# Kernel tuning notes

Hardware: AMD Instinct MI355X
Metric: run time of the kernel (lower is better)

## Reference

```python
import jax, jax.numpy as jnp
import numpy as np

D_MODEL = 1024
NUM_SLOTS = 64
TOP_K = 8
B, T = 4, 4096


def setup_inputs() -> dict:
    key = jax.random.key(0)
    ks = jax.random.split(key, 16)
    D, S = D_MODEL, NUM_SLOTS
    H = D // 2  # route MLP hidden (hardcoded d_model//2 in source)
    sc = lambda fan_in: 1.0 / np.sqrt(fan_in)
    inp = {
        "x": jax.random.normal(ks[0], (B, T, D), dtype=jnp.float32),
        # learned params
        "slot_init": jax.random.normal(ks[1], (S, D), dtype=jnp.float32) * 0.1,
        "slot_scale": jnp.ones((S, 1), dtype=jnp.float32),
        "w1": jax.random.normal(ks[2], (H, 2 * D), dtype=jnp.float32) * sc(2 * D),
        "b1": jnp.zeros((H,), dtype=jnp.float32),
        "w2": jax.random.normal(ks[3], (S, H), dtype=jnp.float32) * sc(H),
        "b2": jnp.zeros((S,), dtype=jnp.float32),
        "gru_wih": jax.random.normal(ks[4], (3 * D, D), dtype=jnp.float32) * sc(D),
        "gru_whh": jax.random.normal(ks[5], (3 * D, D), dtype=jnp.float32) * sc(D),
        "gru_bih": jnp.zeros((3 * D,), dtype=jnp.float32),
        "gru_bhh": jnp.zeros((3 * D,), dtype=jnp.float32),
        "wv": jax.random.normal(ks[6], (D, D), dtype=jnp.float32) * sc(D),
        "bv": jnp.zeros((D,), dtype=jnp.float32),
        "wo": jax.random.normal(ks[7], (D, D), dtype=jnp.float32) * sc(D),
        "bo": jnp.zeros((D,), dtype=jnp.float32),
        "tau": jnp.ones((1,), dtype=jnp.float32),
    }
    return inp


def _forward(x, slot_init, slot_scale, w1, b1, w2, b2,
             gru_wih, gru_whh, gru_bih, gru_bhh, wv, bv, wo, bo, tau):
    Bn, Tn, D = x.shape
    Sn = slot_init.shape[0]
    # initial slot states, expanded over batch: (B, S, D)
    S = jnp.broadcast_to((slot_init * slot_scale)[None], (Bn, Sn, D)).astype(x.dtype)
    slot_mean = S.mean(axis=1, keepdims=True)                      # (B,1,D)
    ctx = jnp.concatenate([x, jnp.broadcast_to(slot_mean, x.shape)], axis=-1)  # (B,T,2D)
    h = jax.nn.gelu(ctx @ w1.T + b1, approximate=False)
    route_logits = (h @ w2.T + b2) / (jnp.abs(tau) + 0.1)          # (B,T,S)
    topk_vals, topk_idx = jax.lax.top_k(route_logits, TOP_K)
    topk_w = jax.nn.softmax(topk_vals, axis=-1)                    # (B,T,K)
    # scatter top-k weights into dense alpha (B,T,S)
    alpha = jnp.sum(topk_w[..., None] * jax.nn.one_hot(topk_idx, Sn, dtype=x.dtype), axis=-2)
    slot_input = jnp.einsum('bts,btd->bsd', alpha, x)              # dispatch
    slot_wsum = alpha.sum(axis=1) + 1e-8                           # (B,S)
    gi = (slot_input / slot_wsum[..., None]).reshape(Bn * Sn, D)
    hs = S.reshape(Bn * Sn, D)
    # GRUCell (torch semantics)
    gx = gi @ gru_wih.T + gru_bih                                  # (BS, 3D)
    gh = hs @ gru_whh.T + gru_bhh
    xr, xz, xn = jnp.split(gx, 3, axis=-1)
    hr, hz, hn = jnp.split(gh, 3, axis=-1)
    r = jax.nn.sigmoid(xr + hr)
    z = jax.nn.sigmoid(xz + hz)
    n = jnp.tanh(xn + r * hn)
    h_new = (1.0 - z) * n + z * hs
    S_new = h_new.reshape(Bn, Sn, D)
    slot_values = S_new @ wv.T + bv                                # (B,S,D)
    out = jnp.einsum('bts,bsd->btd', alpha, slot_values)           # combine
    return out @ wo.T + bo


def reference(x, slot_init, slot_scale, w1, b1, w2, b2,
              gru_wih, gru_whh, gru_bih, gru_bhh, wv, bv, wo, bo, tau):
    return _forward(x, slot_init, slot_scale, w1, b1, w2, b2,
                    gru_wih, gru_whh, gru_bih, gru_bhh, wv, bv, wo, bo, tau)
```

## Files before the change

### kernel.cpp

```cpp
#include <hip/hip_runtime.h>

using u16 = unsigned short;
using u32 = unsigned int;

typedef __attribute__((ext_vector_type(8))) short bf16x8;
typedef __attribute__((ext_vector_type(4))) float f32x4;

#define NTOK 16384

constexpr size_t OFF_FLAG   = 0;
constexpr size_t OFF_FCNT   = 256;
constexpr size_t OFF_M      = 512;
constexpr size_t OFF_B1P64  = 8704;
constexpr size_t OFF_B1P32  = 12800;
constexpr size_t OFF_B2F    = 14848;
constexpr size_t OFF_BIHF   = 15104;
constexpr size_t OFF_BHHF   = 27392;
constexpr size_t OFF_BVF    = 39680;
constexpr size_t OFF_BOF    = 43776;
constexpr size_t OFF_FLAGS  = 47872;
constexpr size_t OFF_HSHI   = 113408;
constexpr size_t OFF_HSLO   = 244480;
constexpr size_t OFF_HSF    = 375552;
constexpr size_t OFF_GH     = 637696;
constexpr size_t OFF_GIHI   = 1424128;
constexpr size_t OFF_GILO   = 1948416;
constexpr size_t OFF_GX     = 2472704;
constexpr size_t OFF_SNHI   = 5618432;
constexpr size_t OFF_SNLO   = 6142720;
constexpr size_t OFF_SVHI   = 6667008;
constexpr size_t OFF_SVLO   = 7191296;
constexpr size_t OFF_SVO    = 7715584;
constexpr size_t OFF_IDX    = 8764160;
constexpr size_t OFF_WGT    = 9288448;
constexpr size_t OFF_LOGITS = 9812736;
constexpr size_t OFF_W1HI   = 14007040;
constexpr size_t OFF_W1LO   = 16104192;
constexpr size_t OFF_W2HI   = 18201344;
constexpr size_t OFF_W2LO   = 18266880;
constexpr size_t OFF_WIHHI  = 18332416;
constexpr size_t OFF_WIHLO  = 24623872;
constexpr size_t OFF_WHHHI  = 30915328;
constexpr size_t OFF_WHHLO  = 37206784;
constexpr size_t OFF_WVHI   = 43498240;
constexpr size_t OFF_WVLO   = 45595392;
constexpr size_t OFF_WOHI   = 47692544;
constexpr size_t OFF_WOLO   = 49789696;
constexpr size_t OFF_HHI    = 51886848;
constexpr size_t OFF_HLO    = 68664064;
constexpr size_t WS_NEED    = 85441280;

__device__ __forceinline__ float bf2f(u16 u) {
  union { u32 i; float f; } c; c.i = ((u32)u) << 16; return c.f;
}
__device__ __forceinline__ u16 f2bf(float f) {
  u32 x = __float_as_uint(f);
  x += 0x7fffu + ((x >> 16) & 1u);
  return (u16)(x >> 16);
}
__device__ __forceinline__ void splitf(float v, u16& hi, u16& lo) {
  hi = f2bf(v);
  lo = f2bf(v - bf2f(hi));
}
__device__ __forceinline__ float rdval(const void* p, int i, int f32m) {
  return f32m ? ((const float*)p)[i] : bf2f(((const u16*)p)[i]);
}
__device__ __forceinline__ void async16(const u16* g, u16* l) {
  __builtin_amdgcn_global_load_lds((const __attribute__((address_space(1))) void*)g,
                                   (__attribute__((address_space(3))) void*)l, 16, 0, 0);
}

__global__ void k_sniff(const u32* __restrict__ w1w, int* __restrict__ flag) {
  int t = threadIdx.x;
  u32 word = w1w[t * 97];
  int ef = (word >> 7) & 0xFF;
  unsigned long long m = __ballot(ef >= 128);
  if (t == 0) flag[0] = (__popcll(m) >= 8) ? 1 : 0;
}

__global__ __launch_bounds__(256) void k_cvt_all(
    const void* __restrict__ w1, const void* __restrict__ w2,
    const void* __restrict__ wih, const void* __restrict__ whh,
    const void* __restrict__ wv, const void* __restrict__ wo,
    const void* __restrict__ b2, const void* __restrict__ bih,
    const void* __restrict__ bhh, const void* __restrict__ bv,
    const void* __restrict__ bo, char* __restrict__ ws,
    const int* __restrict__ flagp)
{
  const int f = *flagp;
  const long long gid = (long long)blockIdx.x * 256 + threadIdx.x;
  const long long C0 = 1048576, C1 = C0 + 32768, C2 = C1 + 3145728,
                  C3 = C2 + 3145728, C4 = C3 + 1048576, C5 = C4 + 1048576;
  if (gid < C5) {
    const void* src; size_t oh, ol; int i;
    if (gid < C0)      { src = w1;  oh = OFF_W1HI;  ol = OFF_W1LO;  i = (int)gid; }
    else if (gid < C1) { src = w2;  oh = OFF_W2HI;  ol = OFF_W2LO;  i = (int)(gid - C0); }
    else if (gid < C2) { src = wih; oh = OFF_WIHHI; ol = OFF_WIHLO; i = (int)(gid - C1); }
    else if (gid < C3) { src = whh; oh = OFF_WHHHI; ol = OFF_WHHLO; i = (int)(gid - C2); }
    else if (gid < C4) { src = wv;  oh = OFF_WVHI;  ol = OFF_WVLO;  i = (int)(gid - C3); }
    else               { src = wo;  oh = OFF_WOHI;  ol = OFF_WOLO;  i = (int)(gid - C4); }
    float v = rdval(src, i, f);
    u16 hi, lo; splitf(v, hi, lo);
    ((u16*)(ws + oh))[i] = hi;
    ((u16*)(ws + ol))[i] = lo;
    return;
  }
  int r = (int)(gid - C5);
  if (r >= 8256) return;
  const void* src; size_t od; int i;
  if (r < 64)        { src = b2;  od = OFF_B2F;  i = r; }
  else if (r < 3136) { src = bih; od = OFF_BIHF; i = r - 64; }
  else if (r < 6208) { src = bhh; od = OFF_BHHF; i = r - 3136; }
  else if (r < 7232) { src = bv;  od = OFF_BVF;  i = r - 6208; }
  else               { src = bo;  od = OFF_BOF;  i = r - 7232; }
  ((float*)(ws + od))[i] = rdval(src, i, f);
}

template<int MODE>
__global__ __launch_bounds__(512, 2) void gemm_bt(
    const u16* __restrict__ Ahi, const u16* __restrict__ Alo,
    const u16* __restrict__ Bhi, const u16* __restrict__ Blo,
    int M, int N, int K, int ldb,
    const float* __restrict__ biasF, float* __restrict__ outF,
    u16* __restrict__ outHi, u16* __restrict__ outLo)
{
  __shared__ alignas(16) u16 smem[2 * 2 * 8192];
  const int t    = threadIdx.x;
  const int grp  = t >> 8;
  const int tl   = t & 255;
  const int wvid = tl >> 6;
  const int lane = t & 63;
  const int quad = lane >> 4;
  const int l16  = lane & 15;
  const int row0 = blockIdx.x * 128;
  const int col0 = blockIdx.y * 128;
  const int wr   = (wvid >> 1) * 64;
  const int wc   = (wvid & 1) * 64;

  const int ra  = tl >> 2;
  const int kqe = (tl & 3) * 8;
  int r_a0 = row0 + ra;      if (r_a0 > M - 1) r_a0 = M - 1;
  int r_a1 = row0 + ra + 64; if (r_a1 > M - 1) r_a1 = M - 1;
  int r_b0 = col0 + ra;      if (r_b0 > N - 1) r_b0 = N - 1;
  int r_b1 = col0 + ra + 64; if (r_b1 > N - 1) r_b1 = N - 1;
  const size_t aoff0 = (size_t)r_a0 * K + kqe;
  const size_t aoff1 = (size_t)r_a1 * K + kqe;
  const size_t boff0 = (size_t)r_b0 * ldb + kqe;
  const size_t boff1 = (size_t)r_b1 * ldb + kqe;

  const int KH  = K >> 1;
  const int NIT = 3 * (KH >> 5);
  int sp = 0, sk = grp * KH;
  const int skend = grp * KH + KH;

  u16* const base = smem + grp * 16384;
  auto stage = [&](int buf) {
    const u16* Ap = (sp == 1) ? Alo : Ahi;
    const u16* Bp = (sp == 2) ? Blo : Bhi;
    u16* At = base + buf * 8192;
    u16* Bt = At + 4096;
    async16(Ap + aoff0 + sk, &At[(wvid * 64) * 8]);
    async16(Ap + aoff1 + sk, &At[(wvid * 64 + 256) * 8]);
    async16(Bp + boff0 + sk, &Bt[(wvid * 64) * 8]);
    async16(Bp + boff1 + sk, &Bt[(wvid * 64 + 256) * 8]);
    sk += 32;
    if (sk == skend) { sk = grp * KH; ++sp; }
  };

  f32x4 acc[4][4] = {};
  stage(0);
  asm volatile("s_waitcnt vmcnt(0)" ::: "memory");
  __syncthreads();
  int cur = 0;
  for (int it = 0; it < NIT; ++it) {
    if (it + 1 < NIT) stage(cur ^ 1);
    const u16* At = base + cur * 8192;
    const u16* Bt = At + 4096;
    bf16x8 af[4], bfr[4];
    #pragma unroll
    for (int mt = 0; mt < 4; ++mt)
      af[mt] = *(const bf16x8*)&At[(wr + mt * 16 + l16) * 32 + quad * 8];
    #pragma unroll
    for (int nt = 0; nt < 4; ++nt)
      bfr[nt] = *(const bf16x8*)&Bt[(wc + nt * 16 + l16) * 32 + quad * 8];
    #pragma unroll
    for (int mt = 0; mt < 4; ++mt)
      #pragma unroll
      for (int nt = 0; nt < 4; ++nt)
        acc[mt][nt] = __builtin_amdgcn_mfma_f32_16x16x32_bf16(
            af[mt], bfr[nt], acc[mt][nt], 0, 0, 0);
    asm volatile("s_waitcnt vmcnt(0)" ::: "memory");
    __syncthreads();
    cur ^= 1;
  }

  float* red = (float*)smem;
  #pragma unroll 1
  for (int half = 0; half < 2; ++half) {
    if (grp == 1 && (wvid & 1) == half) {
      #pragma unroll
      for (int mt = 0; mt < 4; ++mt)
        #pragma unroll
        for (int nt = 0; nt < 4; ++nt)
          #pragma unroll
          for (int r2 = 0; r2 < 4; ++r2)
            red[(wr + mt * 16 + quad * 4 + r2) * 64 + nt * 16 + l16] =
                acc[mt][nt][r2];
    }
    __syncthreads();
    if (grp == 0 && (wvid & 1) == half) {
      #pragma unroll
      for (int mt = 0; mt < 4; ++mt)
        #pragma unroll
        for (int nt = 0; nt < 4; ++nt)
          #pragma unroll
          for (int r2 = 0; r2 < 4; ++r2)
            acc[mt][nt][r2] +=
                red[(wr + mt * 16 + quad * 4 + r2) * 64 + nt * 16 + l16];
    }
    __syncthreads();
  }
  if (grp != 0) return;

  #pragma unroll
  for (int mt = 0; mt < 4; ++mt) {
    #pragma unroll
    for (int nt = 0; nt < 4; ++nt) {
      const int col = col0 + wc + nt * 16 + l16;
      if (col >= N) continue;
      #pragma unroll
      for (int r2 = 0; r2 < 4; ++r2) {
        const int row = row0 + wr + mt * 16 + quad * 4 + r2;
        if (row >= M) continue;
        float v = acc[mt][nt][r2] + biasF[col];
        size_t idx = (size_t)row * N + col;
        if constexpr (MODE == 0) {
          outF[idx] = v;
        } else {
          u16 hi, lo; splitf(v, hi, lo);
          outHi[idx] = hi; outLo[idx] = lo;
        }
      }
    }
  }
}

__global__ __launch_bounds__(256, 4) void gemm_router(
    const void* __restrict__ X,
    const u16* __restrict__ Bhi, const u16* __restrict__ Blo,
    int M, int N, int K, int ldb, const float* __restrict__ biasF,
    u16* __restrict__ outHi, u16* __restrict__ outLo,
    const int* __restrict__ flagp)
{
  __shared__ alignas(16) u16 Athi[64 * 32];
  __shared__ alignas(16) u16 Atlo[64 * 32];
  __shared__ alignas(16) u16 Bthi[128 * 32];
  __shared__ alignas(16) u16 Btlo[128 * 32];
  const int f32m = *flagp;
  const int t    = threadIdx.x;
  const int wvid = t >> 6;
  const int lane = t & 63;
  const int quad = lane >> 4;
  const int l16  = lane & 15;
  const int row0 = blockIdx.x * 64;
  const int col0 = blockIdx.y * 128;
  const int wr   = (wvid >> 1) * 32;
  const int wc   = (wvid & 1) * 64;

  const int ra  = t >> 2;
  const int kqe = (t & 3) * 8;
  int r_b0 = col0 + ra;      if (r_b0 > N - 1) r_b0 = N - 1;
  int r_b1 = col0 + ra + 64; if (r_b1 > N - 1) r_b1 = N - 1;
  const u16* gBhi0 = Bhi + (size_t)r_b0 * ldb + kqe;
  const u16* gBhi1 = Bhi + (size_t)r_b1 * ldb + kqe;
  const u16* gBlo0 = Blo + (size_t)r_b0 * ldb + kqe;
  const u16* gBlo1 = Blo + (size_t)r_b1 * ldb + kqe;
  const float* Xf = (const float*)X;
  const u16*   Xb = (const u16*)X;

  f32x4 acc[2][4] = {};

  for (int k0 = 0; k0 < K; k0 += 32) {
    async16(gBhi0 + k0, &Bthi[(wvid * 64) * 8]);
    async16(gBhi1 + k0, &Bthi[(wvid * 64 + 256) * 8]);
    async16(gBlo0 + k0, &Btlo[(wvid * 64) * 8]);
    async16(gBlo1 + k0, &Btlo[(wvid * 64 + 256) * 8]);
    #pragma unroll
    for (int i = 0; i < 2; ++i) {
      int j = t + 256 * i;
      int row = j >> 3, kq = (j & 7) * 4;
      int grow = row0 + row; if (grow > M - 1) grow = M - 1;
      ushort4 hi4, lo4;
      if (f32m) {
        const float4 v = *(const float4*)(Xf + (size_t)grow * K + k0 + kq);
        splitf(v.x, hi4.x, lo4.x);
        splitf(v.y, hi4.y, lo4.y);
        splitf(v.z, hi4.z, lo4.z);
        splitf(v.w, hi4.w, lo4.w);
      } else {
        hi4 = *(const ushort4*)(Xb + (size_t)grow * K + k0 + kq);
        lo4.x = lo4.y = lo4.z = lo4.w = 0;
      }
      *(ushort4*)&Athi[row * 32 + kq] = hi4;
      *(ushort4*)&Atlo[row * 32 + kq] = lo4;
    }
    asm volatile("s_waitcnt vmcnt(0)" ::: "memory");
    __syncthreads();
    bf16x8 ah[2], al[2], bh[4], bl[4];
    #pragma unroll
    for (int mt = 0; mt < 2; ++mt) {
      ah[mt] = *(const bf16x8*)&Athi[(wr + mt * 16 + l16) * 32 + quad * 8];
      al[mt] = *(const bf16x8*)&Atlo[(wr + mt * 16 + l16) * 32 + quad * 8];
    }
    #pragma unroll
    for (int nt = 0; nt < 4; ++nt) {
      bh[nt] = *(const bf16x8*)&Bthi[(wc + nt * 16 + l16) * 32 + quad * 8];
      bl[nt] = *(const bf16x8*)&Btlo[(wc + nt * 16 + l16) * 32 + quad * 8];
    }
    #pragma unroll
    for (int mt = 0; mt < 2; ++mt)
      #pragma unroll
      for (int nt = 0; nt < 4; ++nt) {
        acc[mt][nt] = __builtin_amdgcn_mfma_f32_16x16x32_bf16(
            ah[mt], bh[nt], acc[mt][nt], 0, 0, 0);
        acc[mt][nt] = __builtin_amdgcn_mfma_f32_16x16x32_bf16(
            al[mt], bh[nt], acc[mt][nt], 0, 0, 0);
        acc[mt][nt] = __builtin_amdgcn_mfma_f32_16x16x32_bf16(
            ah[mt], bl[nt], acc[mt][nt], 0, 0, 0);
      }
    __syncthreads();
  }

  #pragma unroll
  for (int mt = 0; mt < 2; ++mt) {
    #pragma unroll
    for (int nt = 0; nt < 4; ++nt) {
      const int col = col0 + wc + nt * 16 + l16;
      if (col >= N) continue;
      #pragma unroll
      for (int r2 = 0; r2 < 4; ++r2) {
        const int row = row0 + wr + mt * 16 + quad * 4 + r2;
        if (row >= M) continue;
        float v = acc[mt][nt][r2] + biasF[col];
        v = 0.5f * v * (1.0f + erff(v * 0.70710678118654752f));
        u16 hi, lo; splitf(v, hi, lo);
        size_t idx = (size_t)row * N + col;
        outHi[idx] = hi; outLo[idx] = lo;
      }
    }
  }
}

__global__ __launch_bounds__(256) void k_init(const void* __restrict__ sli,
    const void* __restrict__ slsc, const int* __restrict__ flagp,
    double* __restrict__ m64, int* __restrict__ fcnt,
    u16* __restrict__ hshi, u16* __restrict__ hslo, float* __restrict__ hsf)
{
  int f = *flagp;
  int gid = blockIdx.x * 256 + threadIdx.x;
  if (gid == 0) fcnt[0] = 0;
  if (gid < 1024) {
    double s = 0.0;
    for (int j = 0; j < 64; ++j)
      s += (double)rdval(sli, j * 1024 + gid, f) * (double)rdval(slsc, j, f);
    m64[gid] = s * (1.0 / 64.0);
  }
  for (int i = gid; i < 64 * 1024; i += 16384) {
    int s = i >> 10;
    float v = rdval(sli, i, f) * rdval(slsc, s, f);
    splitf(v, hshi[i], hslo[i]);
    hsf[i] = v;
  }
}

__global__ __launch_bounds__(256) void k_b1p(const void* __restrict__ w1,
    const void* __restrict__ b1, const int* __restrict__ flagp,
    const double* __restrict__ m64, double* __restrict__ b1p64,
    float* __restrict__ b1p32)
{
  int f = *flagp;
  int h = blockIdx.x * 256 + threadIdx.x;
  if (h >= 512) return;
  double a = (double)rdval(b1, h, f);
  if (f) {
    const float* wr = (const float*)w1 + (size_t)h * 2048 + 1024;
    for (int d = 0; d < 1024; ++d) a += (double)wr[d] * m64[d];
  } else {
    const u16* wr = (const u16*)w1 + (size_t)h * 2048 + 1024;
    for (int d = 0; d < 1024; ++d) a += (double)bf2f(wr[d]) * m64[d];
  }
  b1p64[h] = a;
  b1p32[h] = (float)a;
}

__global__ __launch_bounds__(256) void k_topk(const float* __restrict__ logits,
    const void* __restrict__ tau, const int* __restrict__ flagp,
    int* __restrict__ idxb, float* __restrict__ wgtb,
    int* __restrict__ fcnt, int* __restrict__ flags)
{
  const int f32m = *flagp;
  const int n    = blockIdx.x * 4 + (threadIdx.x >> 6);
  const int lane = threadIdx.x & 63;
  float cur = logits[(size_t)n * 64 + lane];
  float tv[8]; int ti[8]; float v9 = 0.f;
  #pragma unroll
  for (int it = 0; it < 9; ++it) {
    float v = cur; int i = lane;
    #pragma unroll
    for (int off = 32; off; off >>= 1) {
      float ov = __shfl_xor(v, off);
      int   oi = __shfl_xor(i, off);
      if (ov > v || (ov == v && oi < i)) { v = ov; i = oi; }
    }
    if (it < 8) { tv[it] = v; ti[it] = i; if (lane == i) cur = -__builtin_inff(); }
    else v9 = v;
  }
  float itau = 1.0f / (fabsf(rdval(tau, 0, f32m)) + 0.1f);
  float e[8], z = 0.f;
  #pragma unroll
  for (int k = 0; k < 8; ++k) { e[k] = expf((tv[k] - tv[0]) * itau); z += e[k]; }
  if (lane == 0) {
    float theta = f32m ? 2e-4f : 1e-4f;
    if (tv[7] - v9 < theta) { int p = atomicAdd(fcnt, 1); flags[p] = n; }
    float rz = 1.0f / z;
    #pragma unroll
    for (int k = 0; k < 8; ++k) {
      idxb[n * 8 + k] = ti[k];
      wgtb[n * 8 + k] = e[k] * rz;
    }
  }
}

__global__ __launch_bounds__(256) void k_repair(const void* __restrict__ x,
    const void* __restrict__ w1, const void* __restrict__ w2,
    const void* __restrict__ b2, const void* __restrict__ tau,
    const int* __restrict__ flagp, const double* __restrict__ b1p64,
    const int* __restrict__ fcnt, const int* __restrict__ flags,
    int* __restrict__ idxb, float* __restrict__ wgtb)
{
  __shared__ double hsm[512];
  __shared__ double lg[64];
  const int f = *flagp;
  const int cnt = *fcnt;
  const int t = threadIdx.x;
  for (int q = blockIdx.x; q < cnt; q += gridDim.x) {
    const int n = flags[q];
    for (int h = t; h < 512; h += 256) {
      double a = b1p64[h];
      if (f) {
        const float* xr = (const float*)x + (size_t)n * 1024;
        const float* wr = (const float*)w1 + (size_t)h * 2048;
        for (int d = 0; d < 1024; ++d) a += (double)xr[d] * (double)wr[d];
      } else {
        const u16* xr = (const u16*)x + (size_t)n * 1024;
        const u16* wr = (const u16*)w1 + (size_t)h * 2048;
        for (int d = 0; d < 1024; ++d) a += (double)bf2f(xr[d]) * (double)bf2f(wr[d]);
      }
      hsm[h] = 0.5 * a * (1.0 + erf(a * 0.70710678118654752440));
    }
    __syncthreads();
    if (t < 64) {
      double a = (double)rdval(b2, t, f);
      if (f) {
        const float* wr = (const float*)w2 + (size_t)t * 512;
        for (int k = 0; k < 512; ++k) a += hsm[k] * (double)wr[k];
      } else {
        const u16* wr = (const u16*)w2 + (size_t)t * 512;
        for (int k = 0; k < 512; ++k) a += hsm[k] * (double)bf2f(wr[k]);
      }
      lg[t] = a;
    }
    __syncthreads();
    if (t == 0) {
      double tv = fabs((double)rdval(tau, 0, f)) + 0.1;
      double vals[8]; int ids[8];
      for (int it = 0; it < 8; ++it) {
        double best = -1e300; int bi = 0;
        for (int i = 0; i < 64; ++i)
          if (lg[i] > best) { best = lg[i]; bi = i; }
        vals[it] = best; ids[it] = bi; lg[bi] = -1e300;
      }
      double e[8], z = 0.0;
      for (int k = 0; k < 8; ++k) { e[k] = exp((vals[k] - vals[0]) / tv); z += e[k]; }
      for (int k = 0; k < 8; ++k) {
        idxb[n * 8 + k] = ids[k];
        wgtb[n * 8 + k] = (float)(e[k] / z);
      }
    }
    __syncthreads();
  }
}

__global__ __launch_bounds__(256) void k_dispatch(const void* __restrict__ X,
    const int* __restrict__ flagp, const int* __restrict__ idxb,
    const float* __restrict__ wgtb, u16* __restrict__ gihi, u16* __restrict__ gilo)
{
  __shared__ int   ltok[4096];
  __shared__ float lw[4096];
  __shared__ int   lcnt;
  __shared__ float lws;
  const int f32m = *flagp;
  const int bs = blockIdx.x;
  const int b  = bs >> 6;
  const int s  = bs & 63;
  const int t  = threadIdx.x;
  if (t == 0) { lcnt = 0; lws = 0.f; }
  __syncthreads();
  float mysum = 0.f;
  for (int tok = b * 4096 + t; tok < (b + 1) * 4096; tok += 256) {
    int hit = -1;
    #pragma unroll
    for (int k = 0; k < 8; ++k)
      if (idxb[(size_t)tok * 8 + k] == s) hit = k;
    if (hit >= 0) {
      float w = wgtb[(size_t)tok * 8 + hit];
      int p = atomicAdd(&lcnt, 1);
      ltok[p] = tok; lw[p] = w;
      mysum += w;
    }
  }
  atomicAdd(&lws, mysum);
  __syncthreads();
  const int cnt = lcnt;
  const float inv = 1.0f / (lws + 1e-8f);
  float a0 = 0, a1 = 0, a2 = 0, a3 = 0;
  if (f32m) {
    const float* Xf = (const float*)X;
    for (int e = 0; e < cnt; ++e) {
      int tok = ltok[e]; float w = lw[e];
      const float* xr = Xf + (size_t)tok * 1024;
      a0 += w * xr[t]; a1 += w * xr[t + 256];
      a2 += w * xr[t + 512]; a3 += w * xr[t + 768];
    }
  } else {
    const u16* Xb = (const u16*)X;
    for (int e = 0; e < cnt; ++e) {
      int tok = ltok[e]; float w = lw[e];
      const u16* xr = Xb + (size_t)tok * 1024;
      a0 += w * bf2f(xr[t]); a1 += w * bf2f(xr[t + 256]);
      a2 += w * bf2f(xr[t + 512]); a3 += w * bf2f(xr[t + 768]);
    }
  }
  size_t base = (size_t)bs * 1024;
  splitf(a0 * inv, gihi[base + t],       gilo[base + t]);
  splitf(a1 * inv, gihi[base + t + 256], gilo[base + t + 256]);
  splitf(a2 * inv, gihi[base + t + 512], gilo[base + t + 512]);
  splitf(a3 * inv, gihi[base + t + 768], gilo[base + t + 768]);
}

__global__ __launch_bounds__(256) void k_gru(const float* __restrict__ gx,
    const float* __restrict__ gh, const float* __restrict__ hsf,
    u16* __restrict__ snhi, u16* __restrict__ snlo)
{
  int gid = blockIdx.x * 256 + threadIdx.x;
  int r = gid >> 10, d = gid & 1023, s = r & 63;
  const float* gxr = gx + (size_t)r * 3072;
  const float* ghr = gh + (size_t)s * 3072;
  float rr = 1.0f / (1.0f + expf(-(gxr[d] + ghr[d])));
  float zz = 1.0f / (1.0f + expf(-(gxr[1024 + d] + ghr[1024 + d])));
  float nn = tanhf(gxr[2048 + d] + rr * ghr[2048 + d]);
  float hs = hsf[s * 1024 + d];
  float hv = (1.0f - zz) * nn + zz * hs;
  splitf(hv, snhi[gid], snlo[gid]);
}

__global__ __launch_bounds__(256) void k_out(const int* __restrict__ idxb,
    const float* __restrict__ wgtb, const float* __restrict__ svo,
    const int* __restrict__ flagp, void* __restrict__ out)
{
  const int f32m = *flagp;
  int n = blockIdx.x * 4 + (threadIdx.x >> 6);
  int lane = threadIdx.x & 63;
  int b = n >> 12;
  const float* svb = svo + (size_t)b * 64 * 1024;
  int id[8]; float w[8];
  #pragma unroll
  for (int k = 0; k < 8; ++k) { id[k] = idxb[n * 8 + k]; w[k] = wgtb[n * 8 + k]; }
  #pragma unroll
  for (int i = 0; i < 16; ++i) {
    int d = i * 64 + lane;
    float a = 0.f;
    #pragma unroll
    for (int k = 0; k < 8; ++k) a += w[k] * svb[(size_t)id[k] * 1024 + d];
    size_t idx = (size_t)n * 1024 + d;
    if (f32m) ((float*)out)[idx] = a;
    else      ((u16*)out)[idx] = f2bf(a);
  }
}

extern "C" void kernel_launch(void* const* d_in, const int* in_sizes, int n_in,
                              void* d_out, int out_size, void* d_ws, size_t ws_size,
                              hipStream_t stream) {
  if (ws_size < WS_NEED) {
    hipMemsetAsync(d_out, 0, (size_t)out_size * 2, stream);
    return;
  }
  const void* x    = d_in[0];
  const void* sli  = d_in[1];
  const void* slsc = d_in[2];
  const void* w1   = d_in[3];
  const void* b1   = d_in[4];
  const void* w2   = d_in[5];
  const void* b2   = d_in[6];
  const void* wih  = d_in[7];
  const void* whh  = d_in[8];
  const void* bih  = d_in[9];
  const void* bhh  = d_in[10];
  const void* wv   = d_in[11];
  const void* bv   = d_in[12];
  const void* wo   = d_in[13];
  const void* bo   = d_in[14];
  const void* tau  = d_in[15];
  char* ws = (char*)d_ws;

  int*    flag   = (int*)(ws + OFF_FLAG);
  int*    fcnt   = (int*)(ws + OFF_FCNT);
  double* m64    = (double*)(ws + OFF_M);
  double* b1p64  = (double*)(ws + OFF_B1P64);
  float*  b1p32  = (float*)(ws + OFF_B1P32);
  float*  b2f    = (float*)(ws + OFF_B2F);
  float*  bihf   = (float*)(ws + OFF_BIHF);
  float*  bhhf   = (float*)(ws + OFF_BHHF);
  float*  bvf    = (float*)(ws + OFF_BVF);
  float*  bof    = (float*)(ws + OFF_BOF);
  int*    flags  = (int*)(ws + OFF_FLAGS);
  u16*    hshi   = (u16*)(ws + OFF_HSHI);
  u16*    hslo   = (u16*)(ws + OFF_HSLO);
  float*  hsf    = (float*)(ws + OFF_HSF);
  float*  gh     = (float*)(ws + OFF_GH);
  u16*    gihi   = (u16*)(ws + OFF_GIHI);
  u16*    gilo   = (u16*)(ws + OFF_GILO);
  float*  gx     = (float*)(ws + OFF_GX);
  u16*    snhi   = (u16*)(ws + OFF_SNHI);
  u16*    snlo   = (u16*)(ws + OFF_SNLO);
  u16*    svhi   = (u16*)(ws + OFF_SVHI);
  u16*    svlo   = (u16*)(ws + OFF_SVLO);
  float*  svo    = (float*)(ws + OFF_SVO);
  int*    idxb   = (int*)(ws + OFF_IDX);
  float*  wgtb   = (float*)(ws + OFF_WGT);
  float*  logits = (float*)(ws + OFF_LOGITS);
  u16*    w1hi   = (u16*)(ws + OFF_W1HI);
  u16*    w1lo   = (u16*)(ws + OFF_W1LO);
  u16*    w2hi   = (u16*)(ws + OFF_W2HI);
  u16*    w2lo   = (u16*)(ws + OFF_W2LO);
  u16*    wihhi  = (u16*)(ws + OFF_WIHHI);
  u16*    wihlo  = (u16*)(ws + OFF_WIHLO);
  u16*    whhhi  = (u16*)(ws + OFF_WHHHI);
  u16*    whhlo  = (u16*)(ws + OFF_WHHLO);
  u16*    wvhi   = (u16*)(ws + OFF_WVHI);
  u16*    wvlo   = (u16*)(ws + OFF_WVLO);
  u16*    wohi   = (u16*)(ws + OFF_WOHI);
  u16*    wolo   = (u16*)(ws + OFF_WOLO);
  u16*    hhi    = (u16*)(ws + OFF_HHI);
  u16*    hlo    = (u16*)(ws + OFF_HLO);

  k_sniff<<<1, 64, 0, stream>>>((const u32*)w1, flag);

  k_init<<<64, 256, 0, stream>>>(sli, slsc, flag, m64, fcnt, hshi, hslo, hsf);
  k_b1p<<<2, 256, 0, stream>>>(w1, b1, flag, m64, b1p64, b1p32);

  k_cvt_all<<<37025, 256, 0, stream>>>(w1, w2, wih, whh, wv, wo,
                                       b2, bih, bhh, bv, bo, ws, flag);

  gemm_bt<0><<<dim3(1, 24), 512, 0, stream>>>(
      hshi, hslo, whhhi, whhlo, 64, 3072, 1024, 1024, bhhf, gh, nullptr, nullptr);

  gemm_router<<<dim3(256, 4), 256, 0, stream>>>(
      x, w1hi, w1lo, NTOK, 512, 1024, 2048, b1p32, hhi, hlo, flag);

  gemm_bt<0><<<dim3(128, 1), 512, 0, stream>>>(
      hhi, hlo, w2hi, w2lo, NTOK, 64, 512, 512, b2f, logits, nullptr, nullptr);

  k_topk<<<4096, 256, 0, stream>>>(logits, tau, flag, idxb, wgtb, fcnt, flags);
  k_repair<<<1024, 256, 0, stream>>>(x, w1, w2, b2, tau, flag, b1p64, fcnt, flags,
                                     idxb, wgtb);
  k_dispatch<<<256, 256, 0, stream>>>(x, flag, idxb, wgtb, gihi, gilo);

  gemm_bt<0><<<dim3(2, 24), 512, 0, stream>>>(
      gihi, gilo, wihhi, wihlo, 256, 3072, 1024, 1024, bihf, gx, nullptr, nullptr);

  k_gru<<<1024, 256, 0, stream>>>(gx, gh, hsf, snhi, snlo);

  gemm_bt<3><<<dim3(2, 8), 512, 0, stream>>>(
      snhi, snlo, wvhi, wvlo, 256, 1024, 1024, 1024, bvf, nullptr, svhi, svlo);

  gemm_bt<0><<<dim3(2, 8), 512, 0, stream>>>(
      svhi, svlo, wohi, wolo, 256, 1024, 1024, 1024, bof, svo, nullptr, nullptr);

  k_out<<<4096, 256, 0, stream>>>(idxb, wgtb, svo, flag, d_out);

  (void)in_sizes; (void)n_in; (void)out_size; (void)ws_size;
}
```

Baseline: 791.9 us.

## Split slot dispatch over token chunks with partial sums and a reduce kernel

```diff
diff --git a/kernel.cpp b/kernel.cpp
--- a/kernel.cpp
+++ b/kernel.cpp
@@ -48,7 +48,9 @@
 constexpr size_t OFF_WOLO   = 49789696;
 constexpr size_t OFF_HHI    = 51886848;
 constexpr size_t OFF_HLO    = 68664064;
-constexpr size_t WS_NEED    = 85441280;
+constexpr size_t OFF_DPART  = 85441280;
+constexpr size_t OFF_DWSUM  = 93829888;
+constexpr size_t WS_NEED    = 93838080;
 
 __device__ __forceinline__ float bf2f(u16 u) {
   union { u32 i; float f; } c; c.i = ((u32)u) << 16; return c.f;
@@ -493,21 +495,25 @@
 
 __global__ __launch_bounds__(256) void k_dispatch(const void* __restrict__ X,
     const int* __restrict__ flagp, const int* __restrict__ idxb,
-    const float* __restrict__ wgtb, u16* __restrict__ gihi, u16* __restrict__ gilo)
-{
-  __shared__ int   ltok[4096];
-  __shared__ float lw[4096];
+    const float* __restrict__ wgtb,
+    float* __restrict__ dpart, float* __restrict__ dwsum)
+{
+  __shared__ int   ltok[512];
+  __shared__ float lw[512];
   __shared__ int   lcnt;
   __shared__ float lws;
   const int f32m = *flagp;
-  const int bs = blockIdx.x;
-  const int b  = bs >> 6;
-  const int s  = bs & 63;
-  const int t  = threadIdx.x;
+  const int g     = blockIdx.x;
+  const int s     = g & 63;
+  const int bc    = g >> 6;
+  const int b     = bc >> 3;
+  const int chunk = bc & 7;
+  const int t     = threadIdx.x;
   if (t == 0) { lcnt = 0; lws = 0.f; }
   __syncthreads();
+  const int tok0 = b * 4096 + chunk * 512;
   float mysum = 0.f;
-  for (int tok = b * 4096 + t; tok < (b + 1) * 4096; tok += 256) {
+  for (int tok = tok0 + t; tok < tok0 + 512; tok += 256) {
     int hit = -1;
     #pragma unroll
     for (int k = 0; k < 8; ++k)
@@ -522,30 +528,51 @@
   atomicAdd(&lws, mysum);
   __syncthreads();
   const int cnt = lcnt;
-  const float inv = 1.0f / (lws + 1e-8f);
-  float a0 = 0, a1 = 0, a2 = 0, a3 = 0;
+  float a0 = 0.f, a1 = 0.f, a2 = 0.f, a3 = 0.f;
   if (f32m) {
     const float* Xf = (const float*)X;
     for (int e = 0; e < cnt; ++e) {
       int tok = ltok[e]; float w = lw[e];
-      const float* xr = Xf + (size_t)tok * 1024;
-      a0 += w * xr[t]; a1 += w * xr[t + 256];
-      a2 += w * xr[t + 512]; a3 += w * xr[t + 768];
+      const float4 v = *(const float4*)(Xf + (size_t)tok * 1024 + 4 * t);
+      a0 += w * v.x; a1 += w * v.y; a2 += w * v.z; a3 += w * v.w;
     }
   } else {
     const u16* Xb = (const u16*)X;
     for (int e = 0; e < cnt; ++e) {
       int tok = ltok[e]; float w = lw[e];
-      const u16* xr = Xb + (size_t)tok * 1024;
-      a0 += w * bf2f(xr[t]); a1 += w * bf2f(xr[t + 256]);
-      a2 += w * bf2f(xr[t + 512]); a3 += w * bf2f(xr[t + 768]);
-    }
-  }
-  size_t base = (size_t)bs * 1024;
-  splitf(a0 * inv, gihi[base + t],       gilo[base + t]);
-  splitf(a1 * inv, gihi[base + t + 256], gilo[base + t + 256]);
-  splitf(a2 * inv, gihi[base + t + 512], gilo[base + t + 512]);
-  splitf(a3 * inv, gihi[base + t + 768], gilo[base + t + 768]);
+      const ushort4 v = *(const ushort4*)(Xb + (size_t)tok * 1024 + 4 * t);
+      a0 += w * bf2f(v.x); a1 += w * bf2f(v.y);
+      a2 += w * bf2f(v.z); a3 += w * bf2f(v.w);
+    }
+  }
+  const int bs = b * 64 + s;
+  float* pp = dpart + ((size_t)bs * 8 + chunk) * 1024 + 4 * t;
+  float4 outv = { a0, a1, a2, a3 };
+  *(float4*)pp = outv;
+  if (t == 0) dwsum[bs * 8 + chunk] = lws;
+}
+
+__global__ __launch_bounds__(256) void k_dreduce(const float* __restrict__ dpart,
+    const float* __restrict__ dwsum, u16* __restrict__ gihi, u16* __restrict__ gilo)
+{
+  const int bs = blockIdx.x;
+  const int t  = threadIdx.x;
+  float ws = 0.f;
+  #pragma unroll
+  for (int c = 0; c < 8; ++c) ws += dwsum[bs * 8 + c];
+  const float inv = 1.0f / (ws + 1e-8f);
+  float a0 = 0.f, a1 = 0.f, a2 = 0.f, a3 = 0.f;
+  const float* pb = dpart + (size_t)bs * 8 * 1024 + 4 * t;
+  #pragma unroll
+  for (int c = 0; c < 8; ++c) {
+    const float4 v = *(const float4*)(pb + c * 1024);
+    a0 += v.x; a1 += v.y; a2 += v.z; a3 += v.w;
+  }
+  const size_t base = (size_t)bs * 1024 + 4 * t;
+  splitf(a0 * inv, gihi[base + 0], gilo[base + 0]);
+  splitf(a1 * inv, gihi[base + 1], gilo[base + 1]);
+  splitf(a2 * inv, gihi[base + 2], gilo[base + 2]);
+  splitf(a3 * inv, gihi[base + 3], gilo[base + 3]);
 }
 
 __global__ __launch_bounds__(256) void k_gru(const float* __restrict__ gx,
@@ -653,6 +680,8 @@
   u16*    wolo   = (u16*)(ws + OFF_WOLO);
   u16*    hhi    = (u16*)(ws + OFF_HHI);
   u16*    hlo    = (u16*)(ws + OFF_HLO);
+  float*  dpart  = (float*)(ws + OFF_DPART);
+  float*  dwsum  = (float*)(ws + OFF_DWSUM);
 
   k_sniff<<<1, 64, 0, stream>>>((const u32*)w1, flag);
 
@@ -674,7 +703,8 @@
   k_topk<<<4096, 256, 0, stream>>>(logits, tau, flag, idxb, wgtb, fcnt, flags);
   k_repair<<<1024, 256, 0, stream>>>(x, w1, w2, b2, tau, flag, b1p64, fcnt, flags,
                                      idxb, wgtb);
-  k_dispatch<<<256, 256, 0, stream>>>(x, flag, idxb, wgtb, gihi, gilo);
+  k_dispatch<<<2048, 256, 0, stream>>>(x, flag, idxb, wgtb, dpart, dwsum);
+  k_dreduce<<<256, 256, 0, stream>>>(dpart, dwsum, gihi, gilo);
 
   gemm_bt<0><<<dim3(2, 24), 512, 0, stream>>>(
       gihi, gilo, wihhi, wihlo, 256, 3072, 1024, 1024, bihf, gx, nullptr, nullptr);
```

Measured after the change: 769.1 us. -2.9%, faster.
